# Performance work log

Hardware: AMD Instinct MI355X
Metric: run time of the kernel (lower is better)

## Reference

```python
import jax, jax.numpy as jnp
import numpy as np

K = 3        # kernel_size
PAD = 1      # padding
STRIDE = 1   # stride (must be 1: module asserts offset HxW == input HxW)
DIL = 1      # dilation


def _bilinear_gather(x, py, px):
    """x: (B,C,H,W); py,px: (B,KK,Ho,Wo) float sample coords.
    Returns (B,C,KK,Ho,Wo), zero outside bounds (DCNv2 semantics)."""
    B, C, H, W = x.shape
    y0 = jnp.floor(py); x0 = jnp.floor(px)
    wy1 = py - y0; wy0 = 1.0 - wy1
    wx1 = px - x0; wx0 = 1.0 - wx1
    flat = x.reshape(B, C, H * W)

    def gather(yi, xi):
        valid = (yi >= 0) & (yi < H) & (xi >= 0) & (xi < W)
        yc = jnp.clip(yi, 0, H - 1).astype(jnp.int32)
        xc = jnp.clip(xi, 0, W - 1).astype(jnp.int32)
        idx = (yc * W + xc).reshape(B, 1, -1)                      # (B,1,KK*Ho*Wo)
        g = jnp.take_along_axis(flat, jnp.broadcast_to(idx, (B, C, idx.shape[-1])), axis=2)
        g = g.reshape(B, C, *yi.shape[1:])                          # (B,C,KK,Ho,Wo)
        return jnp.where(valid[:, None], g, 0.0)

    v00 = gather(y0, x0)
    v01 = gather(y0, x0 + 1)
    v10 = gather(y0 + 1, x0)
    v11 = gather(y0 + 1, x0 + 1)
    wy0 = wy0[:, None]; wy1 = wy1[:, None]; wx0 = wx0[:, None]; wx1 = wx1[:, None]
    return wy0 * (wx0 * v00 + wx1 * v01) + wy1 * (wx0 * v10 + wx1 * v11)


def dcn_v2(x, coord_offset, coord_weight, weight, bias):
    B, C, H, W = x.shape
    O = weight.shape[0]
    KK = K * K
    # offset channels ordered (k, [y,x]) per DCNv2 layout
    offs = coord_offset.reshape(B, KK, 2, H, W)
    oy, ox = offs[:, :, 0], offs[:, :, 1]
    ky, kx = jnp.meshgrid(jnp.arange(K), jnp.arange(K), indexing='ij')
    ky = ky.reshape(KK); kx = kx.reshape(KK)
    # base sampling grid for each output pixel / kernel tap: (KK,H,W)
    py = (jnp.arange(H) * STRIDE - PAD)[None, :, None] + (ky * DIL)[:, None, None]
    px = (jnp.arange(W) * STRIDE - PAD)[None, None, :] + (kx * DIL)[:, None, None]
    py = py.astype(x.dtype)[None] + oy   # (B,KK,H,W)
    px = px.astype(x.dtype)[None] + ox
    sampled = _bilinear_gather(x, py, px)              # (B,C,KK,H,W)
    sampled = sampled * coord_weight[:, None]          # modulation mask
    out = jnp.einsum('bckhw,ock->bohw', sampled, weight.reshape(O, C, KK))
    return out + bias[None, :, None, None]


def setup_inputs() -> dict:
    key = jax.random.key(0)
    k1, k2, k3, k4, k5 = jax.random.split(key, 5)
    B, C, O, H, W = 8, 256, 256, 64, 64
    return {
        'input': jax.random.normal(k1, (B, C, H, W), dtype=jnp.float32),
        'coord_offset': jax.random.normal(k2, (B, 2 * K * K, H, W), dtype=jnp.float32),
        'coord_weight': jax.random.uniform(k3, (B, K * K, H, W), dtype=jnp.float32),
        'weight': jax.random.normal(k4, (O, C, K, K), dtype=jnp.float32) * 0.02,
        'bias': jax.random.normal(k5, (O,), dtype=jnp.float32) * 0.01,
    }


def reference(input, coord_offset, coord_weight, weight, bias):
    return dcn_v2(input, coord_offset, coord_weight, weight, bias)
```

## Files before the change

### kernel.cpp

```cpp
#include <hip/hip_runtime.h>
#include <hip/hip_bf16.h>
#include <stdint.h>

typedef _Float16 f16_t;
typedef f16_t f16x8 __attribute__((ext_vector_type(8)));
typedef float f32x4 __attribute__((ext_vector_type(4)));

__device__ inline void lgkm_barrier() {
    __builtin_amdgcn_s_waitcnt(0xC07F);
    __builtin_amdgcn_s_barrier();
}

__global__ __launch_bounds__(256) void k_prep(const float* __restrict__ x,
                                              const float* __restrict__ w,
                                              f16_t* __restrict__ xt,
                                              f16_t* __restrict__ Wp) {
    __shared__ __align__(16) char smem[36864];
    const int t = threadIdx.x;
    if (blockIdx.x < 512) {
        f16_t* tT = (f16_t*)smem;
        const int b = blockIdx.x >> 6;
        const int y = blockIdx.x & 63;
        const float* src = x + ((size_t)(b * 256) * 64 + y) * 64;
        const int x4 = (t & 15) * 4;
        const int cs = t >> 4;
#pragma unroll
        for (int cc = 0; cc < 256; cc += 16) {
            const int c = cc + cs;
            float4 v = *(const float4*)(src + (size_t)c * 4096 + x4);
            const int chunk = c >> 3, e = c & 7;
#pragma unroll
            for (int j = 0; j < 4; ++j) {
                const int xx = x4 + j;
                const float f = (j == 0) ? v.x : (j == 1) ? v.y : (j == 2) ? v.z : v.w;
                tT[xx * 256 + ((chunk ^ (xx & 31)) << 3) + e] = (f16_t)f;
            }
        }
        __syncthreads();
        f16_t* dst = xt + ((size_t)(b * 64 + y) * 64) * 256;
#pragma unroll
        for (int i = 0; i < 8; ++i) {
            const int s = t + 256 * i;
            const int xx = s >> 5, cg = s & 31;
            *(f16x8*)(dst + xx * 256 + cg * 8) =
                *(const f16x8*)(tT + xx * 256 + ((cg ^ (xx & 31)) << 3));
        }
    } else {
        float* lw = (float*)smem;
        const int o0 = (blockIdx.x - 512) * 4;
        const float4* src = (const float4*)(w + (size_t)o0 * 2304);
#pragma unroll
        for (int i = 0; i < 9; ++i)
            ((float4*)lw)[t + 256 * i] = src[t + 256 * i];
        __syncthreads();
#pragma unroll
        for (int i = 0; i < 5; ++i) {
            const int u = t + 256 * i;
            if (u < 1152) {
                const int o = u / 288, r = u - o * 288;
                const int kb2 = r >> 3, rr = r & 7;
                const int s = rr >> 2, qq = rr & 3;
                const int kk = kb2 >> 2, cp = kb2 & 3;
                f16x8 v;
#pragma unroll
                for (int e = 0; e < 8; ++e) {
                    const int c = cp * 64 + s * 32 + qq * 8 + e;
                    v[e] = (f16_t)lw[o * 2304 + c * 9 + kk];
                }
                *(f16x8*)(Wp + ((size_t)(kb2 * 2 + s) * 256 + o0 + o) * 32 + qq * 8) = v;
            }
        }
    }
}

__global__ __launch_bounds__(512, 4) void k_dcn(
    const f16_t* __restrict__ xt, const f16_t* __restrict__ Wp,
    const float* __restrict__ coff, const float* __restrict__ cwm,
    const float* __restrict__ bias, float* __restrict__ out) {

    __shared__ __align__(16) f16_t sS[2][64 * 64];
    __shared__ __align__(16) int2 sT[9 * 64 * 4];

    const int blk = blockIdx.x;
    const int b  = blk & 7;
    const int h  = blk >> 3;
    const int t = threadIdx.x;
    const int wv = t >> 6;
    const int lane = t & 63;

    const int p = t >> 3;
    const int q = t & 7;

    const int fr = lane & 15;
    const int quad = lane >> 4;
    const int swz = fr & 7;

    for (int u = t; u < 576; u += 512) {
        const int kk = u >> 6, wpx = u & 63;
        float oy = coff[((size_t)(b * 18 + kk * 2 + 0) * 64 + h) * 64 + wpx];
        float ox = coff[((size_t)(b * 18 + kk * 2 + 1) * 64 + h) * 64 + wpx];
        float m  = cwm [((size_t)(b * 9 + kk) * 64 + h) * 64 + wpx];
        float py = (float)(h - 1 + (kk / 3)) + oy;
        float px = (float)(wpx - 1 + (kk % 3)) + ox;
        float fy = floorf(py), fx = floorf(px);
        int y0 = (int)fy, x0 = (int)fx;
        int y1 = y0 + 1,  x1 = x0 + 1;
        float wy1 = py - fy, wx1 = px - fx;
        float wy0 = 1.0f - wy1, wx0 = 1.0f - wx1;
        bool vy0 = (y0 >= 0) && (y0 < 64), vy1 = (y1 >= 0) && (y1 < 64);
        bool vx0 = (x0 >= 0) && (x0 < 64), vx1 = (x1 >= 0) && (x1 < 64);
        int yc0 = min(max(y0, 0), 63), yc1 = min(max(y1, 0), 63);
        int xc0 = min(max(x0, 0), 63), xc1 = min(max(x1, 0), 63);
        const int base = b * 4096;
        float cw[4];
        int   ca[4];
        cw[0] = (vy0 && vx0) ? wy0 * wx0 * m : 0.0f;
        cw[1] = (vy0 && vx1) ? wy0 * wx1 * m : 0.0f;
        cw[2] = (vy1 && vx0) ? wy1 * wx0 * m : 0.0f;
        cw[3] = (vy1 && vx1) ? wy1 * wx1 * m : 0.0f;
        ca[0] = (base + yc0 * 64 + xc0) * 512;
        ca[1] = (base + yc0 * 64 + xc1) * 512;
        ca[2] = (base + yc1 * 64 + xc0) * 512;
        ca[3] = (base + yc1 * 64 + xc1) * 512;
#pragma unroll
        for (int c = 0; c < 4; ++c) {
            unsigned short ws = __builtin_bit_cast(unsigned short, (f16_t)cw[c]);
            sT[(kk * 64 + wpx) * 4 + c] = make_int2(ca[c], (int)ws);
        }
    }
    __syncthreads();

    const f16_t* wA = Wp + (wv * 32 + fr) * 32 + quad * 8;
    f16_t* const swb0 = &sS[0][p * 64 + ((q ^ (p & 7)) * 8)];
    const int qb = q * 16;

    f32x4 acc[2][4] = {};
    f16x8 aC[2][2], aN[2][2];

    auto loadA = [&](int it, f16x8 (&a)[2][2]) {
        const f16_t* wn = wA + (size_t)it * 16384;
        a[0][0] = *(const f16x8*)(wn);
        a[0][1] = *(const f16x8*)(wn + 8192);
        a[1][0] = *(const f16x8*)(wn + 512);
        a[1][1] = *(const f16x8*)(wn + 8192 + 512);
    };

    auto do_mfma = [&](int cur) {
        const f16_t* sb = &sS[cur][0];
#pragma unroll
        for (int s = 0; s < 2; ++s) {
            const int coffe = ((s * 4 + quad) ^ swz) * 8;
            f16x8 bb[4];
#pragma unroll
            for (int nt = 0; nt < 4; ++nt)
                bb[nt] = *(const f16x8*)(sb + (nt * 16 + fr) * 64 + coffe);
#pragma unroll
            for (int mt = 0; mt < 2; ++mt)
#pragma unroll
                for (int nt = 0; nt < 4; ++nt)
                    acc[mt][nt] = __builtin_amdgcn_mfma_f32_16x16x32_f16(
                        aC[mt][s], bb[nt], acc[mt][nt], 0, 0, 0);
        }
    };

    auto sample_into = [&](int it, int buf) {
        const int kk = it >> 2, cp = it & 3;
        const int4* tp = (const int4*)&sT[(kk * 64 + p) * 4];
        int4 t0 = tp[0], t1 = tp[1];
        const int cb = cp * 128 + qb;
        const char* xb = (const char*)xt;
        f16x8 g0 = *(const f16x8*)(xb + (t0.x + cb));
        f16x8 g1 = *(const f16x8*)(xb + (t0.z + cb));
        f16x8 g2 = *(const f16x8*)(xb + (t1.x + cb));
        f16x8 g3 = *(const f16x8*)(xb + (t1.z + cb));
        f16_t w0 = __builtin_bit_cast(f16_t, (unsigned short)t0.y);
        f16_t w1 = __builtin_bit_cast(f16_t, (unsigned short)t0.w);
        f16_t w2 = __builtin_bit_cast(f16_t, (unsigned short)t1.y);
        f16_t w3 = __builtin_bit_cast(f16_t, (unsigned short)t1.w);
        f16x8 w0v = {w0, w0, w0, w0, w0, w0, w0, w0};
        f16x8 w1v = {w1, w1, w1, w1, w1, w1, w1, w1};
        f16x8 w2v = {w2, w2, w2, w2, w2, w2, w2, w2};
        f16x8 w3v = {w3, w3, w3, w3, w3, w3, w3, w3};
        f16x8 ov = g0 * w0v + g1 * w1v + g2 * w2v + g3 * w3v;
        *(f16x8*)(swb0 + buf * 4096) = ov;
    };

    sample_into(0, 0);
    loadA(0, aC);
    lgkm_barrier();

#pragma unroll 2
    for (int it = 0; it < 36; ++it) {
        const int cur = it & 1;
        if (it < 35) {
            sample_into(it + 1, 1 - cur);
            loadA(it + 1, aN);
            do_mfma(cur);
#pragma unroll
            for (int mt = 0; mt < 2; ++mt)
#pragma unroll
                for (int s = 0; s < 2; ++s) aC[mt][s] = aN[mt][s];
        } else {
            do_mfma(cur);
        }
        lgkm_barrier();
    }

    const int rowq = quad * 4;
#pragma unroll
    for (int mt = 0; mt < 2; ++mt) {
#pragma unroll
        for (int r = 0; r < 4; ++r) {
            const int og = wv * 32 + mt * 16 + rowq + r;
            const float bs = bias[og];
            float* opn = out + ((size_t)(b * 256 + og) * 64 + h) * 64;
#pragma unroll
            for (int nt = 0; nt < 4; ++nt) {
                opn[nt * 16 + fr] = acc[mt][nt][r] + bs;
            }
        }
    }
}

extern "C" void kernel_launch(void* const* d_in, const int* in_sizes, int n_in,
                              void* d_out, int out_size, void* d_ws, size_t ws_size,
                              hipStream_t stream) {
    const float* x    = (const float*)d_in[0];
    const float* coff = (const float*)d_in[1];
    const float* cwm  = (const float*)d_in[2];
    const float* wgt  = (const float*)d_in[3];
    const float* bias = (const float*)d_in[4];
    float* out = (float*)d_out;

    f16_t* xt = (f16_t*)d_ws;
    f16_t* Wp = xt + (size_t)8 * 64 * 64 * 256;

    k_prep<<<576, 256, 0, stream>>>(x, wgt, xt, Wp);
    k_dcn <<<512, 512, 0, stream>>>(xt, Wp, coff, cwm, bias, out);
}
```

Measured before the change: 149.1 us.

## Retile MFMA warps to 64x32 tiles, split gather/combine, simplify prep transpose

The main kernel now tiles each wave as 4 M-tiles by 2 N-tiles instead of 2x4, so each wave loads more weight fragments but fewer shared-memory B fragments per step. The bilinear sampling is split into a gather phase issued before the MFMAs and a combine/write phase after, so global gather latency can overlap with the matrix math. Sample-table reads are now done only once per kernel tap. The A-operand prefetch double buffer is dropped in favour of loading at the top of each iteration, which may expose weight load latency. The prep kernel uses 512 threads and writes the transposed fp16 layout directly from registers instead of staging through LDS.

```diff
diff --git a/kernel.cpp b/kernel.cpp
--- a/kernel.cpp
+++ b/kernel.cpp
@@ -11,63 +11,58 @@
     __builtin_amdgcn_s_barrier();
 }
 
-__global__ __launch_bounds__(256) void k_prep(const float* __restrict__ x,
+__global__ __launch_bounds__(512) void k_prep(const float* __restrict__ x,
                                               const float* __restrict__ w,
                                               f16_t* __restrict__ xt,
                                               f16_t* __restrict__ Wp) {
-    __shared__ __align__(16) char smem[36864];
+    __shared__ __align__(16) float lw[9216];
     const int t = threadIdx.x;
     if (blockIdx.x < 512) {
-        f16_t* tT = (f16_t*)smem;
         const int b = blockIdx.x >> 6;
         const int y = blockIdx.x & 63;
         const float* src = x + ((size_t)(b * 256) * 64 + y) * 64;
         const int x4 = (t & 15) * 4;
-        const int cs = t >> 4;
-#pragma unroll
-        for (int cc = 0; cc < 256; cc += 16) {
-            const int c = cc + cs;
-            float4 v = *(const float4*)(src + (size_t)c * 4096 + x4);
-            const int chunk = c >> 3, e = c & 7;
-#pragma unroll
-            for (int j = 0; j < 4; ++j) {
-                const int xx = x4 + j;
-                const float f = (j == 0) ? v.x : (j == 1) ? v.y : (j == 2) ? v.z : v.w;
-                tT[xx * 256 + ((chunk ^ (xx & 31)) << 3) + e] = (f16_t)f;
+        const int c0 = (t >> 4) * 8;
+        float4 v[8];
+#pragma unroll
+        for (int e = 0; e < 8; ++e)
+            v[e] = *(const float4*)(src + (size_t)(c0 + e) * 4096 + x4);
+        f16_t* dst = xt + ((size_t)(b * 64 + y) * 64) * 256;
+#pragma unroll
+        for (int j = 0; j < 4; ++j) {
+            f16x8 o;
+#pragma unroll
+            for (int e = 0; e < 8; ++e) {
+                const float f = (j == 0) ? v[e].x : (j == 1) ? v[e].y
+                              : (j == 2) ? v[e].z : v[e].w;
+                o[e] = (f16_t)f;
             }
+            *(f16x8*)(dst + (x4 + j) * 256 + c0) = o;
+        }
+    } else {
+        const int o0 = (blockIdx.x - 512) * 4;
+        const float4* srcw = (const float4*)(w + (size_t)o0 * 2304);
+#pragma unroll
+        for (int i = 0; i < 5; ++i) {
+            const int idx = t + 512 * i;
+            if (idx < 2304) ((float4*)lw)[idx] = srcw[idx];
         }
         __syncthreads();
-        f16_t* dst = xt + ((size_t)(b * 64 + y) * 64) * 256;
-#pragma unroll
-        for (int i = 0; i < 8; ++i) {
-            const int s = t + 256 * i;
-            const int xx = s >> 5, cg = s & 31;
-            *(f16x8*)(dst + xx * 256 + cg * 8) =
-                *(const f16x8*)(tT + xx * 256 + ((cg ^ (xx & 31)) << 3));
-        }
-    } else {
-        float* lw = (float*)smem;
-        const int o0 = (blockIdx.x - 512) * 4;
-        const float4* src = (const float4*)(w + (size_t)o0 * 2304);
-#pragma unroll
-        for (int i = 0; i < 9; ++i)
-            ((float4*)lw)[t + 256 * i] = src[t + 256 * i];
-        __syncthreads();
-#pragma unroll
-        for (int i = 0; i < 5; ++i) {
-            const int u = t + 256 * i;
+#pragma unroll
+        for (int i = 0; i < 3; ++i) {
+            const int u = t + 512 * i;
             if (u < 1152) {
                 const int o = u / 288, r = u - o * 288;
                 const int kb2 = r >> 3, rr = r & 7;
                 const int s = rr >> 2, qq = rr & 3;
                 const int kk = kb2 >> 2, cp = kb2 & 3;
-                f16x8 v;
+                f16x8 vv;
 #pragma unroll
                 for (int e = 0; e < 8; ++e) {
                     const int c = cp * 64 + s * 32 + qq * 8 + e;
-                    v[e] = (f16_t)lw[o * 2304 + c * 9 + kk];
+                    vv[e] = (f16_t)lw[o * 2304 + c * 9 + kk];
                 }
-                *(f16x8*)(Wp + ((size_t)(kb2 * 2 + s) * 256 + o0 + o) * 32 + qq * 8) = v;
+                *(f16x8*)(Wp + ((size_t)(kb2 * 2 + s) * 256 + o0 + o) * 32 + qq * 8) = vv;
             }
         }
     }
@@ -87,6 +82,8 @@
     const int t = threadIdx.x;
     const int wv = t >> 6;
     const int lane = t & 63;
+    const int mg = wv >> 1;
+    const int ng = wv & 1;
 
     const int p = t >> 3;
     const int q = t & 7;
@@ -130,49 +127,40 @@
     }
     __syncthreads();
 
-    const f16_t* wA = Wp + (wv * 32 + fr) * 32 + quad * 8;
+    const f16_t* wA = Wp + (mg * 64 + fr) * 32 + quad * 8;
     f16_t* const swb0 = &sS[0][p * 64 + ((q ^ (p & 7)) * 8)];
     const int qb = q * 16;
-
-    f32x4 acc[2][4] = {};
-    f16x8 aC[2][2], aN[2][2];
-
-    auto loadA = [&](int it, f16x8 (&a)[2][2]) {
+    const char* xb = (const char*)xt;
+
+    f32x4 acc[4][2] = {};
+    f16x8 aC[4][2];
+    f16x8 g0, g1, g2, g3;
+    int4 t0, t1;
+
+    auto loadA = [&](int it) {
         const f16_t* wn = wA + (size_t)it * 16384;
-        a[0][0] = *(const f16x8*)(wn);
-        a[0][1] = *(const f16x8*)(wn + 8192);
-        a[1][0] = *(const f16x8*)(wn + 512);
-        a[1][1] = *(const f16x8*)(wn + 8192 + 512);
-    };
-
-    auto do_mfma = [&](int cur) {
-        const f16_t* sb = &sS[cur][0];
-#pragma unroll
-        for (int s = 0; s < 2; ++s) {
-            const int coffe = ((s * 4 + quad) ^ swz) * 8;
-            f16x8 bb[4];
-#pragma unroll
-            for (int nt = 0; nt < 4; ++nt)
-                bb[nt] = *(const f16x8*)(sb + (nt * 16 + fr) * 64 + coffe);
-#pragma unroll
-            for (int mt = 0; mt < 2; ++mt)
-#pragma unroll
-                for (int nt = 0; nt < 4; ++nt)
-                    acc[mt][nt] = __builtin_amdgcn_mfma_f32_16x16x32_f16(
-                        aC[mt][s], bb[nt], acc[mt][nt], 0, 0, 0);
-        }
-    };
-
-    auto sample_into = [&](int it, int buf) {
+#pragma unroll
+        for (int mt = 0; mt < 4; ++mt) {
+            aC[mt][0] = *(const f16x8*)(wn + mt * 512);
+            aC[mt][1] = *(const f16x8*)(wn + 8192 + mt * 512);
+        }
+    };
+
+    auto gather_issue = [&](int it) {
         const int kk = it >> 2, cp = it & 3;
-        const int4* tp = (const int4*)&sT[(kk * 64 + p) * 4];
-        int4 t0 = tp[0], t1 = tp[1];
+        if ((it & 3) == 0) {
+            const int4* tp = (const int4*)&sT[(kk * 64 + p) * 4];
+            t0 = tp[0];
+            t1 = tp[1];
+        }
         const int cb = cp * 128 + qb;
-        const char* xb = (const char*)xt;
-        f16x8 g0 = *(const f16x8*)(xb + (t0.x + cb));
-        f16x8 g1 = *(const f16x8*)(xb + (t0.z + cb));
-        f16x8 g2 = *(const f16x8*)(xb + (t1.x + cb));
-        f16x8 g3 = *(const f16x8*)(xb + (t1.z + cb));
+        g0 = *(const f16x8*)(xb + (t0.x + cb));
+        g1 = *(const f16x8*)(xb + (t0.z + cb));
+        g2 = *(const f16x8*)(xb + (t1.x + cb));
+        g3 = *(const f16x8*)(xb + (t1.z + cb));
+    };
+
+    auto combine_write = [&](int buf) {
         f16_t w0 = __builtin_bit_cast(f16_t, (unsigned short)t0.y);
         f16_t w1 = __builtin_bit_cast(f16_t, (unsigned short)t0.w);
         f16_t w2 = __builtin_bit_cast(f16_t, (unsigned short)t1.y);
@@ -185,21 +173,36 @@
         *(f16x8*)(swb0 + buf * 4096) = ov;
     };
 
-    sample_into(0, 0);
-    loadA(0, aC);
+    auto do_mfma = [&](int cur) {
+        const f16_t* sb = &sS[cur][ng * 2048];
+#pragma unroll
+        for (int s = 0; s < 2; ++s) {
+            const int coffe = ((s * 4 + quad) ^ swz) * 8;
+            f16x8 bb[2];
+#pragma unroll
+            for (int nt = 0; nt < 2; ++nt)
+                bb[nt] = *(const f16x8*)(sb + (nt * 16 + fr) * 64 + coffe);
+#pragma unroll
+            for (int mt = 0; mt < 4; ++mt)
+#pragma unroll
+                for (int nt = 0; nt < 2; ++nt)
+                    acc[mt][nt] = __builtin_amdgcn_mfma_f32_16x16x32_f16(
+                        aC[mt][s], bb[nt], acc[mt][nt], 0, 0, 0);
+        }
+    };
+
+    gather_issue(0);
+    combine_write(0);
     lgkm_barrier();
 
 #pragma unroll 2
     for (int it = 0; it < 36; ++it) {
         const int cur = it & 1;
+        loadA(it);
         if (it < 35) {
-            sample_into(it + 1, 1 - cur);
-            loadA(it + 1, aN);
+            gather_issue(it + 1);
             do_mfma(cur);
-#pragma unroll
-            for (int mt = 0; mt < 2; ++mt)
-#pragma unroll
-                for (int s = 0; s < 2; ++s) aC[mt][s] = aN[mt][s];
+            combine_write(1 - cur);
         } else {
             do_mfma(cur);
         }
@@ -208,14 +211,14 @@
 
     const int rowq = quad * 4;
 #pragma unroll
-    for (int mt = 0; mt < 2; ++mt) {
+    for (int mt = 0; mt < 4; ++mt) {
 #pragma unroll
         for (int r = 0; r < 4; ++r) {
-            const int og = wv * 32 + mt * 16 + rowq + r;
+            const int og = mg * 64 + mt * 16 + rowq + r;
             const float bs = bias[og];
-            float* opn = out + ((size_t)(b * 256 + og) * 64 + h) * 64;
-#pragma unroll
-            for (int nt = 0; nt < 4; ++nt) {
+            float* opn = out + ((size_t)(b * 256 + og) * 64 + h) * 64 + ng * 32;
+#pragma unroll
+            for (int nt = 0; nt < 2; ++nt) {
                 opn[nt * 16 + fr] = acc[mt][nt][r] + bs;
             }
         }
@@ -235,6 +238,6 @@
     f16_t* xt = (f16_t*)d_ws;
     f16_t* Wp = xt + (size_t)8 * 64 * 64 * 256;
 
-    k_prep<<<576, 256, 0, stream>>>(x, wgt, xt, Wp);
+    k_prep<<<576, 512, 0, stream>>>(x, wgt, xt, Wp);
     k_dcn <<<512, 512, 0, stream>>>(xt, Wp, coff, cwm, bias, out);
 }
```

After: 235.3 us. 57.8% more time.
